# Performance work log

Hardware: AMD Instinct MI355X
Metric: run time of the kernel (lower is better)

## Reference

```python
import jax, jax.numpy as jnp
import numpy as np

DIM = 1024
HEADS = 16
DIM_HEAD = 64
INNER = HEADS * DIM_HEAD  # 1024
SCALE = DIM_HEAD ** -0.5


def setup_inputs() -> dict:
    key = jax.random.key(0)
    k1, k2, k3, k4 = jax.random.split(key, 4)
    B, N = 2, 2048
    x = jax.random.normal(k1, (B, N, DIM), dtype=jnp.float32)
    # to_qkv: Linear(dim, 3*inner_dim, bias=False); weight stored as [out, in] in torch,
    # here as [in, out] for x @ W.
    w_qkv = jax.random.normal(k2, (DIM, 3 * INNER), dtype=jnp.float32) * (DIM ** -0.5)
    # to_out: Linear(inner_dim, dim) with bias
    w_out = jax.random.normal(k3, (INNER, DIM), dtype=jnp.float32) * (INNER ** -0.5)
    b_out = jax.random.normal(k4, (DIM,), dtype=jnp.float32) * 0.02
    return {"x": x, "w_qkv": w_qkv, "w_out": w_out, "b_out": b_out}


def reference(x, w_qkv, w_out, b_out):
    B, N, _ = x.shape
    qkv = x @ w_qkv                                  # [B, N, 3*INNER]
    q, k, v = jnp.split(qkv, 3, axis=-1)             # each [B, N, INNER]
    def to_heads(t):
        return t.reshape(B, N, HEADS, DIM_HEAD).transpose(0, 2, 1, 3)  # [B,H,N,D]
    q, k, v = to_heads(q), to_heads(k), to_heads(v)
    dots = jnp.einsum('bhnd,bhmd->bhnm', q, k) * SCALE  # [B,H,N,N]
    attn = jax.nn.softmax(dots, axis=-1)
    out = jnp.einsum('bhnm,bhmd->bhnd', attn, v)        # [B,H,N,D]
    out = out.transpose(0, 2, 1, 3).reshape(B, N, INNER)
    return out @ w_out + b_out
```

## Files before the change

### kernel.cpp

```cpp
#include <hip/hip_runtime.h>
#include <hip/hip_bf16.h>
#include <stdint.h>

#define PDIM   1024
#define HEADS  16
#define DHEAD  64
#define BATCH  2
#define SEQ    2048
#define ROWS   (BATCH*SEQ)
#define NBH    (BATCH*HEADS)

typedef __attribute__((ext_vector_type(8))) short s8v;
typedef __attribute__((ext_vector_type(4))) float f32x4;
typedef __attribute__((ext_vector_type(16))) float f32x16;
typedef unsigned short ushort_t;
typedef unsigned int   uint32;

#define QSCALE 0.18033688011112042f
#define MFIX 12.0f

__device__ __forceinline__ ushort_t f2bf(float x){
  union { float f; uint32 u; } v; v.f = x;
  uint32 r = v.u + 0x7FFFu + ((v.u >> 16) & 1u);
  return (ushort_t)(r >> 16);
}
__device__ __forceinline__ uint32 cvt_pk_bf16(float lo, float hi){
  uint32 r;
  asm("v_cvt_pk_bf16_f32 %0, %1, %2" : "=v"(r) : "v"(lo), "v"(hi));
  return r;
}

typedef const __attribute__((address_space(1))) void* gas_ptr;
typedef __attribute__((address_space(3))) void*       las_ptr;
__device__ __forceinline__ void g2l16(const void* g, void* l){
  __builtin_amdgcn_global_load_lds((gas_ptr)g, (las_ptr)l, 16, 0, 0);
}

__global__ __launch_bounds__(256) void k_prep(
    const float* __restrict__ x, const float* __restrict__ w_qkv,
    const float* __restrict__ w_out,
    ushort_t* __restrict__ Xh, ushort_t* __restrict__ Wqt_h,
    ushort_t* __restrict__ Wot_h){
  __shared__ float tile[64][65];
  const int bid = blockIdx.x;
  if (bid < 4096){
    int i = bid * 256 + threadIdx.x;
    float4 v = reinterpret_cast<const float4*>(x)[i];
    reinterpret_cast<ushort4*>(Xh)[i] =
        make_ushort4(f2bf(v.x), f2bf(v.y), f2bf(v.z), f2bf(v.w));
    return;
  }
  const float* src; ushort_t* dst; int R, C, cb, rb;
  if (bid < 4864){
    int t = bid - 4096; src = w_qkv; dst = Wqt_h; R = 1024; C = 3072;
    cb = (t % 48) * 64; rb = (t / 48) * 64;
  } else {
    int t = bid - 4864; src = w_out; dst = Wot_h; R = 1024; C = 1024;
    cb = (t % 16) * 64; rb = (t / 16) * 64;
  }
  int t = threadIdx.x;
  int lw = t >> 6, lc = t & 63;
#pragma unroll
  for (int i = 0; i < 16; i++){
    int r = i * 4 + lw;
    tile[r][lc] = src[(size_t)(rb + r) * C + cb + lc];
  }
  __syncthreads();
#pragma unroll
  for (int i = 0; i < 16; i++){
    int c = i * 4 + lw;
    dst[(size_t)(cb + c) * R + rb + lc] = f2bf(tile[lc][c]);
  }
}

#define GBM 128
#define GBN 128
#define GBK 64

__global__ __launch_bounds__(256, 2) void k_gemm_qkv(
    const ushort_t* __restrict__ Xh, const ushort_t* __restrict__ Wqt_h,
    ushort_t* __restrict__ Qh, ushort_t* __restrict__ Kh, ushort_t* __restrict__ Vth){
  __shared__ __align__(16) ushort_t Asm[2][GBM * GBK];
  __shared__ __align__(16) ushort_t Bsm[2][GBM * GBK];
  const int tid  = threadIdx.x;
  const int wave = tid >> 6, lane = tid & 63;
  const int mb = blockIdx.y * GBM, nb = blockIdx.x * GBN;
  const int wr = wave >> 1, wc = wave & 1;
  const int l15 = lane & 15, l4 = lane >> 4;
  const int rsub = lane >> 3;
  const int schunk = ((lane & 7) ^ rsub) * 8;
  f32x4 acc[4][4] = {};

  auto stage = [&](int buf, int kb){
    int k0 = kb * GBK;
#pragma unroll
    for (int i = 0; i < 4; i++){
      int row = (i * 4 + wave) * 8 + rsub;
      g2l16(Xh    + (size_t)(mb + row) * 1024 + k0 + schunk, &Asm[buf][(i * 4 + wave) * 512]);
      g2l16(Wqt_h + (size_t)(nb + row) * 1024 + k0 + schunk, &Bsm[buf][(i * 4 + wave) * 512]);
    }
  };

  stage(0, 0);

  for (int kb = 0; kb < 16; kb++){
    const int cur = kb & 1;
    if (kb < 15){
      stage(cur ^ 1, kb + 1);
      asm volatile("s_waitcnt vmcnt(8)" ::: "memory");
    } else {
      asm volatile("s_waitcnt vmcnt(0)" ::: "memory");
    }
    __builtin_amdgcn_s_barrier();
    __builtin_amdgcn_s_setprio(1);
#pragma unroll
    for (int ks = 0; ks < 2; ks++){
      s8v af[4], bfr[4];
#pragma unroll
      for (int f = 0; f < 4; f++){
        int ch = (((ks * 4 + l4) ^ (l15 & 7)) << 3);
        af[f]  = *reinterpret_cast<const s8v*>(&Asm[cur][(wr * 64 + f * 16 + l15) * 64 + ch]);
        bfr[f] = *reinterpret_cast<const s8v*>(&Bsm[cur][(wc * 64 + f * 16 + l15) * 64 + ch]);
      }
#pragma unroll
      for (int fr = 0; fr < 4; fr++)
#pragma unroll
        for (int fc = 0; fc < 4; fc++)
          acc[fr][fc] = __builtin_amdgcn_mfma_f32_16x16x32_bf16(af[fr], bfr[fc], acc[fr][fc], 0, 0, 0);
    }
    __builtin_amdgcn_s_setprio(0);
    __builtin_amdgcn_s_barrier();
  }

  const int pnum = nb >> 10;
#pragma unroll
  for (int fr = 0; fr < 4; fr++){
    int row  = mb + wr * 64 + fr * 16 + l4 * 4;
    int b    = row >> 11;
    int nseq = row & 2047;
#pragma unroll
    for (int fc = 0; fc < 4; fc++){
      int col = nb + wc * 64 + fc * 16 + l15;
      int rem = col & 1023;
      int h = rem >> 6, d = rem & 63;
      int bh = b * 16 + h;
      if (pnum == 0){
        size_t base = ((size_t)bh * SEQ + nseq) * 64 + d;
#pragma unroll
        for (int r = 0; r < 4; r++)
          Qh[base + (size_t)r * 64] = f2bf(acc[fr][fc][r] * QSCALE);
      } else if (pnum == 1){
        size_t base = ((size_t)bh * SEQ + nseq) * 64 + d;
#pragma unroll
        for (int r = 0; r < 4; r++)
          Kh[base + (size_t)r * 64] = f2bf(acc[fr][fc][r]);
      } else {
        size_t base = ((size_t)bh * 64 + d) * SEQ + nseq;
        *reinterpret_cast<ushort4*>(&Vth[base]) =
            make_ushort4(f2bf(acc[fr][fc][0]), f2bf(acc[fr][fc][1]),
                         f2bf(acc[fr][fc][2]), f2bf(acc[fr][fc][3]));
      }
    }
  }
}

__global__ __launch_bounds__(256, 2) void k_gemm_out(
    const ushort_t* __restrict__ Ah, const ushort_t* __restrict__ Bth,
    float* __restrict__ C, const float* __restrict__ bias){
  __shared__ __align__(16) ushort_t Asm[2][GBM * GBK];
  __shared__ __align__(16) ushort_t Bsm[2][GBM * GBK];
  const int tid  = threadIdx.x;
  const int wave = tid >> 6, lane = tid & 63;
  const int mb = blockIdx.y * GBM, nb = blockIdx.x * GBN;
  const int wr = wave >> 1, wc = wave & 1;
  const int l15 = lane & 15, l4 = lane >> 4;
  const int rsub = lane >> 3;
  const int schunk = ((lane & 7) ^ rsub) * 8;
  f32x4 acc[4][4] = {};

  auto stage = [&](int buf, int kb){
    int k0 = kb * GBK;
#pragma unroll
    for (int i = 0; i < 4; i++){
      int row = (i * 4 + wave) * 8 + rsub;
      g2l16(Ah  + (size_t)(mb + row) * 1024 + k0 + schunk, &Asm[buf][(i * 4 + wave) * 512]);
      g2l16(Bth + (size_t)(nb + row) * 1024 + k0 + schunk, &Bsm[buf][(i * 4 + wave) * 512]);
    }
  };

  stage(0, 0);

  for (int kb = 0; kb < 16; kb++){
    const int cur = kb & 1;
    if (kb < 15){
      stage(cur ^ 1, kb + 1);
      asm volatile("s_waitcnt vmcnt(8)" ::: "memory");
    } else {
      asm volatile("s_waitcnt vmcnt(0)" ::: "memory");
    }
    __builtin_amdgcn_s_barrier();
    __builtin_amdgcn_s_setprio(1);
#pragma unroll
    for (int ks = 0; ks < 2; ks++){
      s8v af[4], bfr[4];
#pragma unroll
      for (int f = 0; f < 4; f++){
        int ch = (((ks * 4 + l4) ^ (l15 & 7)) << 3);
        af[f]  = *reinterpret_cast<const s8v*>(&Asm[cur][(wr * 64 + f * 16 + l15) * 64 + ch]);
        bfr[f] = *reinterpret_cast<const s8v*>(&Bsm[cur][(wc * 64 + f * 16 + l15) * 64 + ch]);
      }
#pragma unroll
      for (int fr = 0; fr < 4; fr++)
#pragma unroll
        for (int fc = 0; fc < 4; fc++)
          acc[fr][fc] = __builtin_amdgcn_mfma_f32_16x16x32_bf16(af[fr], bfr[fc], acc[fr][fc], 0, 0, 0);
    }
    __builtin_amdgcn_s_setprio(0);
    __builtin_amdgcn_s_barrier();
  }
#pragma unroll
  for (int fr = 0; fr < 4; fr++){
    int row = mb + wr * 64 + fr * 16 + l4 * 4;
#pragma unroll
    for (int fc = 0; fc < 4; fc++){
      int col = nb + wc * 64 + fc * 16 + l15;
      float bv = bias[col];
#pragma unroll
      for (int r = 0; r < 4; r++)
        C[(size_t)(row + r) * 1024 + col] = acc[fr][fc][r] + bv;
    }
  }
}

__global__ __launch_bounds__(256, 2) void k_flash(
    const ushort_t* __restrict__ Qh, const ushort_t* __restrict__ Kh,
    const ushort_t* __restrict__ Vth, ushort_t* __restrict__ Ah){
  __shared__ __align__(16) ushort_t KhS[2][64 * 64];
  __shared__ __align__(16) ushort_t VhS[2][64 * 64];
  const int lid = blockIdx.x;
  const int xcd = lid & 7, g = lid >> 3;
  const int bh = xcd * 4 + (g & 3);
  const int qb = (g >> 2) * 128;
  const int tid = threadIdx.x, wave = tid >> 6, lane = tid & 63;
  const int l31 = lane & 31, hh = lane >> 5;
  const int b = bh >> 4, hd = bh & 15;
  const size_t hbase = (size_t)bh * SEQ * 64;
  const int rsub = lane >> 3;
  const int schunk = ((lane & 7) ^ rsub) * 8;

  int fch[4];
#pragma unroll
  for (int s = 0; s < 4; s++)
    fch[s] = (((2 * s + hh) ^ (l31 & 7)) << 3);
  const int fbase = l31 * 64;

  s8v qf[4];
#pragma unroll
  for (int s = 0; s < 4; s++)
    qf[s] = *reinterpret_cast<const s8v*>(
        &Qh[hbase + (size_t)(qb + wave * 32 + l31) * 64 + s * 16 + hh * 8]);

  f32x16 o0 = {}, o1 = {};
  float lsum = 0.f;

  auto stage = [&](int buf, int kt){
    int kvb = kt * 64;
#pragma unroll
    for (int i = 0; i < 2; i++){
      int row = (i * 4 + wave) * 8 + rsub;
      g2l16(Kh  + hbase + (size_t)(kvb + row) * 64 + schunk, &KhS[buf][(i * 4 + wave) * 512]);
      g2l16(Vth + ((size_t)bh * 64 + row) * SEQ + kvb + schunk, &VhS[buf][(i * 4 + wave) * 512]);
    }
  };

  stage(0, 0);

  for (int kt = 0; kt < 32; kt++){
    const int cur = kt & 1;
    if (kt < 31){
      stage(cur ^ 1, kt + 1);
      asm volatile("s_waitcnt vmcnt(4)" ::: "memory");
    } else {
      asm volatile("s_waitcnt vmcnt(0)" ::: "memory");
    }
    __builtin_amdgcn_s_barrier();

    f32x16 s0 = {}, s1 = {};
    __builtin_amdgcn_s_setprio(1);
#pragma unroll
    for (int s = 0; s < 4; s++){
      s8v kf0 = *reinterpret_cast<const s8v*>(&KhS[cur][fbase + fch[s]]);
      s8v kf1 = *reinterpret_cast<const s8v*>(&KhS[cur][fbase + 2048 + fch[s]]);
      s0 = __builtin_amdgcn_mfma_f32_32x32x16_bf16(kf0, qf[s], s0, 0, 0, 0);
      s1 = __builtin_amdgcn_mfma_f32_32x32x16_bf16(kf1, qf[s], s1, 0, 0, 0);
    }
    __builtin_amdgcn_s_setprio(0);

    uint32 w[2][8];
#pragma unroll
    for (int t = 0; t < 8; t++){
      float pa = __builtin_amdgcn_exp2f(s0[2 * t]     - MFIX);
      float pb = __builtin_amdgcn_exp2f(s0[2 * t + 1] - MFIX);
      lsum += pa + pb;
      w[0][t] = cvt_pk_bf16(pa, pb);
    }
#pragma unroll
    for (int t = 0; t < 8; t++){
      float pa = __builtin_amdgcn_exp2f(s1[2 * t]     - MFIX);
      float pb = __builtin_amdgcn_exp2f(s1[2 * t + 1] - MFIX);
      lsum += pa + pb;
      w[1][t] = cvt_pk_bf16(pa, pb);
    }

    __builtin_amdgcn_s_setprio(1);
#pragma unroll
    for (int s = 0; s < 4; s++){
      const int rb = s >> 1, u = (s & 1) * 4;
      uint32 m0 = w[rb][u],     m2 = w[rb][u + 2];
      uint32 m1 = w[rb][u + 1], m3 = w[rb][u + 3];
      asm("v_permlane32_swap_b32 %0, %1" : "+v"(m0), "+v"(m2));
      asm("v_permlane32_swap_b32 %0, %1" : "+v"(m1), "+v"(m3));
      union { uint32 u4[4]; s8v v; } pf;
      pf.u4[0] = m0; pf.u4[1] = m1; pf.u4[2] = m2; pf.u4[3] = m3;
      s8v vf0 = *reinterpret_cast<const s8v*>(&VhS[cur][fbase + fch[s]]);
      s8v vf1 = *reinterpret_cast<const s8v*>(&VhS[cur][fbase + 2048 + fch[s]]);
      o0 = __builtin_amdgcn_mfma_f32_32x32x16_bf16(pf.v, vf0, o0, 0, 0, 0);
      o1 = __builtin_amdgcn_mfma_f32_32x32x16_bf16(pf.v, vf1, o1, 0, 0, 0);
    }
    __builtin_amdgcn_s_setprio(0);
    __builtin_amdgcn_s_barrier();
  }

  lsum += __shfl_xor(lsum, 32);
  float linv = 1.f / lsum;
#pragma unroll
  for (int r = 0; r < 16; r++){
    int q = (r & 3) + 8 * (r >> 2) + 4 * hh;
    float sc = __shfl(linv, q);
    int n = qb + wave * 32 + q;
    size_t rowb = (size_t)(b * SEQ + n) * 1024 + hd * 64;
    Ah[rowb + l31]      = f2bf(o0[r] * sc);
    Ah[rowb + 32 + l31] = f2bf(o1[r] * sc);
  }
}

extern "C" void kernel_launch(void* const* d_in, const int* in_sizes, int n_in,
                              void* d_out, int out_size, void* d_ws, size_t ws_size,
                              hipStream_t stream){
  const float* x     = (const float*)d_in[0];
  const float* w_qkv = (const float*)d_in[1];
  const float* w_out = (const float*)d_in[2];
  const float* b_out = (const float*)d_in[3];
  float* out = (float*)d_out;
  char* ws = (char*)d_ws;

  ushort_t* Xh    = (ushort_t*)(ws);
  ushort_t* Wqt_h = (ushort_t*)(ws + 8388608);
  ushort_t* Wot_h = (ushort_t*)(ws + 14680064);
  ushort_t* Qh    = (ushort_t*)(ws + 16777216);
  ushort_t* Kh    = (ushort_t*)(ws + 25165824);
  ushort_t* Vth   = (ushort_t*)(ws + 33554432);
  ushort_t* Ah    = (ushort_t*)(ws + 41943040);

  k_prep<<<5120, 256, 0, stream>>>(x, w_qkv, w_out, Xh, Wqt_h, Wot_h);
  k_gemm_qkv<<<dim3(24, 32), 256, 0, stream>>>(Xh, Wqt_h, Qh, Kh, Vth);
  k_flash<<<512, 256, 0, stream>>>(Qh, Kh, Vth, Ah);
  k_gemm_out<<<dim3(8, 32), 256, 0, stream>>>(Ah, Wot_h, out, b_out);
}
```

Measured before the change: 115.7 us.

## Fold Q scale into weights, compute softmax row sums via MFMA

Folds the query scale into the bf16-converted Q columns of the QKV weight during prep, which removes the per-element multiply in the QKV GEMM epilogue. The attention kernel drops its scalar row-sum accumulation of exponentials and instead gets row sums from an extra MFMA of the probability tile against a ones vector. This also takes out the final shuffle. The first QK MFMA now starts from a zero constant rather than a zeroed accumulator, and the QKV GEMM launch bounds are raised to request 3 blocks per CU. The trade is roughly 50% more PV MFMA work and added accumulator registers, in exchange for fewer VALU adds. The row sums are now built from bf16-rounded probabilities.

```diff
diff --git a/kernel.cpp b/kernel.cpp
--- a/kernel.cpp
+++ b/kernel.cpp
@@ -51,9 +51,11 @@
     return;
   }
   const float* src; ushort_t* dst; int R, C, cb, rb;
+  float scl = 1.f;
   if (bid < 4864){
     int t = bid - 4096; src = w_qkv; dst = Wqt_h; R = 1024; C = 3072;
     cb = (t % 48) * 64; rb = (t / 48) * 64;
+    if (cb < 1024) scl = QSCALE;
   } else {
     int t = bid - 4864; src = w_out; dst = Wot_h; R = 1024; C = 1024;
     cb = (t % 16) * 64; rb = (t / 16) * 64;
@@ -69,7 +71,7 @@
 #pragma unroll
   for (int i = 0; i < 16; i++){
     int c = i * 4 + lw;
-    dst[(size_t)(cb + c) * R + rb + lc] = f2bf(tile[lc][c]);
+    dst[(size_t)(cb + c) * R + rb + lc] = f2bf(tile[lc][c] * scl);
   }
 }
 
@@ -77,7 +79,7 @@
 #define GBN 128
 #define GBK 64
 
-__global__ __launch_bounds__(256, 2) void k_gemm_qkv(
+__global__ __launch_bounds__(256, 3) void k_gemm_qkv(
     const ushort_t* __restrict__ Xh, const ushort_t* __restrict__ Wqt_h,
     ushort_t* __restrict__ Qh, ushort_t* __restrict__ Kh, ushort_t* __restrict__ Vth){
   __shared__ __align__(16) ushort_t Asm[2][GBM * GBK];
@@ -148,7 +150,7 @@
         size_t base = ((size_t)bh * SEQ + nseq) * 64 + d;
 #pragma unroll
         for (int r = 0; r < 4; r++)
-          Qh[base + (size_t)r * 64] = f2bf(acc[fr][fc][r] * QSCALE);
+          Qh[base + (size_t)r * 64] = f2bf(acc[fr][fc][r]);
       } else if (pnum == 1){
         size_t base = ((size_t)bh * SEQ + nseq) * 64 + d;
 #pragma unroll
@@ -260,8 +262,13 @@
     qf[s] = *reinterpret_cast<const s8v*>(
         &Qh[hbase + (size_t)(qb + wave * 32 + l31) * 64 + s * 16 + hh * 8]);
 
+  s8v onesv;
+#pragma unroll
+  for (int j = 0; j < 8; j++) onesv[j] = (short)0x3F80;
+
+  const f32x16 fzero = {};
   f32x16 o0 = {}, o1 = {};
-  float lsum = 0.f;
+  f32x16 o_l = {};
 
   auto stage = [&](int buf, int kt){
     int kvb = kt * 64;
@@ -285,14 +292,17 @@
     }
     __builtin_amdgcn_s_barrier();
 
-    f32x16 s0 = {}, s1 = {};
     __builtin_amdgcn_s_setprio(1);
-#pragma unroll
-    for (int s = 0; s < 4; s++){
-      s8v kf0 = *reinterpret_cast<const s8v*>(&KhS[cur][fbase + fch[s]]);
-      s8v kf1 = *reinterpret_cast<const s8v*>(&KhS[cur][fbase + 2048 + fch[s]]);
-      s0 = __builtin_amdgcn_mfma_f32_32x32x16_bf16(kf0, qf[s], s0, 0, 0, 0);
-      s1 = __builtin_amdgcn_mfma_f32_32x32x16_bf16(kf1, qf[s], s1, 0, 0, 0);
+    s8v kf0 = *reinterpret_cast<const s8v*>(&KhS[cur][fbase + fch[0]]);
+    s8v kg0 = *reinterpret_cast<const s8v*>(&KhS[cur][fbase + 2048 + fch[0]]);
+    f32x16 s0 = __builtin_amdgcn_mfma_f32_32x32x16_bf16(kf0, qf[0], fzero, 0, 0, 0);
+    f32x16 s1 = __builtin_amdgcn_mfma_f32_32x32x16_bf16(kg0, qf[0], fzero, 0, 0, 0);
+#pragma unroll
+    for (int s = 1; s < 4; s++){
+      s8v kf = *reinterpret_cast<const s8v*>(&KhS[cur][fbase + fch[s]]);
+      s8v kg = *reinterpret_cast<const s8v*>(&KhS[cur][fbase + 2048 + fch[s]]);
+      s0 = __builtin_amdgcn_mfma_f32_32x32x16_bf16(kf, qf[s], s0, 0, 0, 0);
+      s1 = __builtin_amdgcn_mfma_f32_32x32x16_bf16(kg, qf[s], s1, 0, 0, 0);
     }
     __builtin_amdgcn_s_setprio(0);
 
@@ -301,14 +311,12 @@
     for (int t = 0; t < 8; t++){
       float pa = __builtin_amdgcn_exp2f(s0[2 * t]     - MFIX);
       float pb = __builtin_amdgcn_exp2f(s0[2 * t + 1] - MFIX);
-      lsum += pa + pb;
       w[0][t] = cvt_pk_bf16(pa, pb);
     }
 #pragma unroll
     for (int t = 0; t < 8; t++){
       float pa = __builtin_amdgcn_exp2f(s1[2 * t]     - MFIX);
       float pb = __builtin_amdgcn_exp2f(s1[2 * t + 1] - MFIX);
-      lsum += pa + pb;
       w[1][t] = cvt_pk_bf16(pa, pb);
     }
 
@@ -324,19 +332,18 @@
       pf.u4[0] = m0; pf.u4[1] = m1; pf.u4[2] = m2; pf.u4[3] = m3;
       s8v vf0 = *reinterpret_cast<const s8v*>(&VhS[cur][fbase + fch[s]]);
       s8v vf1 = *reinterpret_cast<const s8v*>(&VhS[cur][fbase + 2048 + fch[s]]);
-      o0 = __builtin_amdgcn_mfma_f32_32x32x16_bf16(pf.v, vf0, o0, 0, 0, 0);
-      o1 = __builtin_amdgcn_mfma_f32_32x32x16_bf16(pf.v, vf1, o1, 0, 0, 0);
+      o0  = __builtin_amdgcn_mfma_f32_32x32x16_bf16(pf.v, vf0,   o0,  0, 0, 0);
+      o1  = __builtin_amdgcn_mfma_f32_32x32x16_bf16(pf.v, vf1,   o1,  0, 0, 0);
+      o_l = __builtin_amdgcn_mfma_f32_32x32x16_bf16(pf.v, onesv, o_l, 0, 0, 0);
     }
     __builtin_amdgcn_s_setprio(0);
     __builtin_amdgcn_s_barrier();
   }
 
-  lsum += __shfl_xor(lsum, 32);
-  float linv = 1.f / lsum;
 #pragma unroll
   for (int r = 0; r < 16; r++){
+    float sc = 1.f / o_l[r];
     int q = (r & 3) + 8 * (r >> 2) + 4 * hh;
-    float sc = __shfl(linv, q);
     int n = qb + wave * 32 + q;
     size_t rowb = (size_t)(b * SEQ + n) * 1024 + hd * 64;
     Ah[rowb + l31]      = f2bf(o0[r] * sc);
```

Result: no change. 116.3 us (+0.5%).
